# Optimization experiments

Measured on AMD Instinct MI355X. Metric: run time of the kernel, lower is better.

## Reference

```python
import jax, jax.numpy as jnp
import numpy as np

NHEAD = 6
EPS = 1.1920929e-07  # torch RMSNorm default eps = finfo(float32).eps


def _rms(x, g):
    return x * jax.lax.rsqrt(jnp.mean(x * x, axis=-1, keepdims=True) + EPS) * g


def _mha(q, k, v):
    # q: [B, Sq, Hq, D]; k, v: [B, Sk, Hk, D] with Hk == Hq or Hk == 1 (broadcast)
    d = q.shape[-1]
    qh = q.transpose(0, 2, 1, 3)            # [B, Hq, Sq, D]
    kh = k.transpose(0, 2, 1, 3)            # [B, Hk, Sk, D]
    vh = v.transpose(0, 2, 1, 3)
    s = jnp.matmul(qh, kh.transpose(0, 1, 3, 2)) * (1.0 / np.sqrt(d).astype(np.float32))
    a = jax.nn.softmax(s, axis=-1)
    return jnp.matmul(a, vh).transpose(0, 2, 1, 3)  # [B, Sq, Hq, D]


def setup_inputs() -> dict:
    key = jax.random.key(0)
    B, R, G, E, L = 4, 1024, 8, 192, 4
    F = 2 * E  # dim_feedforward = emsize * 2
    ks = jax.random.split(key, 12)

    def w(k, shape):
        return jax.random.normal(k, shape, jnp.float32) * 0.02

    return {
        "hidden": jax.random.normal(ks[0], (B, R, G, E), jnp.float32),
        "Wq1": w(ks[1], (L, E, E)), "Wk1": w(ks[2], (L, E, E)),
        "Wv1": w(ks[3], (L, E, E)), "Wo1": w(ks[4], (L, E, E)),
        "Wq2": w(ks[5], (L, E, E)), "Wk2": w(ks[6], (L, E, E)),
        "Wv2": w(ks[7], (L, E, E)), "Wo2": w(ks[8], (L, E, E)),
        "W1": w(ks[9], (L, E, F)), "W2": w(ks[10], (L, F, E)),
        "g1": jnp.ones((L, E), jnp.float32),
        "g2": jnp.ones((L, E), jnp.float32),
        "g3": jnp.ones((L, E), jnp.float32),
        "single_eval_pos": 768,
    }


def reference(hidden, Wq1, Wk1, Wv1, Wo1, Wq2, Wk2, Wv2, Wo2, W1, W2, g1, g2, g3, single_eval_pos):
    B, R, G, E = hidden.shape
    H, D = NHEAD, E // NHEAD
    sep = int(single_eval_pos)
    L = Wq1.shape[0]
    x = hidden
    for i in range(L):
        # --- per-sample attention between feature groups: seqs of length G ---
        xf = x.reshape(B * R, G, E)
        q = (xf @ Wq1[i]).reshape(B * R, G, H, D)
        k = (xf @ Wk1[i]).reshape(B * R, G, H, D)
        v = (xf @ Wv1[i]).reshape(B * R, G, H, D)
        xf = xf + _mha(q, k, v).reshape(B * R, G, E) @ Wo1[i]
        # --- along-column attention over rows with train/test split ---
        xr = _rms(xf, g1[i]).reshape(B, R, G, E).transpose(0, 2, 1, 3).reshape(B * G, R, E)
        q = (xr @ Wq2[i]).reshape(B * G, R, H, D)
        k = (xr[:, :sep] @ Wk2[i]).reshape(B * G, sep, H, D)
        v = (xr[:, :sep] @ Wv2[i]).reshape(B * G, sep, H, D)
        train_out = _mha(q[:, :sep], k, v)
        # test rows attend to first head's keys/values only (broadcast over heads)
        test_out = _mha(q[:, sep:], k[:, :, :1], v[:, :, :1])
        attn = jnp.concatenate([train_out, test_out], axis=1).reshape(B * G, R, E) @ Wo2[i]
        xc = _rms(xr + attn, g2[i])
        # --- MLP (exact GELU) + final RMSNorm ---
        x = xc.reshape(B, G, R, E).transpose(0, 2, 1, 3)
        x = x + jax.nn.gelu(x @ W1[i], approximate=False) @ W2[i]
        x = _rms(x, g3[i])
    return x
```

## Files before the change

### kernel.cpp

```cpp
#include <hip/hip_runtime.h>
#include <hip/hip_bf16.h>
#include <math.h>

#define B_ 4
#define R_ 1024
#define G_ 8
#define E_ 192
#define H_ 6
#define D_ 32
#define L_ 4
#define F_ 384
#define M_ (B_*R_*G_)
static const size_t NBUF = (size_t)M_ * E_;
static const size_t WPL  = 8 * (size_t)E_ * E_ + 2 * (size_t)E_ * F_;

typedef __attribute__((ext_vector_type(8))) short bf16x8;
typedef __attribute__((ext_vector_type(8))) unsigned short u16x8;
typedef __attribute__((ext_vector_type(4))) float f32x4;

__device__ __forceinline__ float gelu_exact(float x) {
    return 0.5f * x * (1.0f + erff(x * 0.7071067811865475f));
}
__device__ __forceinline__ unsigned short f2bf(float f) {
    __hip_bfloat16 h = __float2bfloat16(f);
    return *(unsigned short*)&h;
}
__device__ __forceinline__ float bf2f(unsigned short h) {
    union { unsigned u; float f; } v; v.u = ((unsigned)h) << 16; return v.f;
}
__device__ __forceinline__ bf16x8 mk8(unsigned long long lo, unsigned long long hi) {
    union { unsigned long long q[2]; bf16x8 v; } u;
    u.q[0] = lo; u.q[1] = hi; return u.v;
}

__global__ __launch_bounds__(256)
void k_convw_all(const float* __restrict__ Wq1, const float* __restrict__ Wk1,
                 const float* __restrict__ Wv1, const float* __restrict__ Wo1,
                 const float* __restrict__ Wq2, const float* __restrict__ Wk2,
                 const float* __restrict__ Wv2, const float* __restrict__ Wo2,
                 const float* __restrict__ W1,  const float* __restrict__ W2,
                 unsigned short* __restrict__ Wt)
{
    const int t = blockIdx.x;
    const int layer = t / 432;
    const int r = t % 432;
    const float* src; unsigned short* dst; int K, N; float scale = 1.f; int tile;
    if (r < 288) {
        const int w = r / 36; tile = r % 36; K = E_; N = E_;
        const float* tab[8] = {Wq1, Wk1, Wv1, Wo1, Wq2, Wk2, Wv2, Wo2};
        src = tab[w] + (size_t)layer * E_ * E_;
        dst = Wt + (size_t)layer * WPL + (size_t)w * E_ * E_;
        if (w == 0) scale = 0.17677669529663687f;
        if (w == 4) scale = 0.17677669529663687f * 1.4426950408889634f;
    } else if (r < 360) {
        tile = r - 288; K = E_; N = F_;
        src = W1 + (size_t)layer * E_ * F_;
        dst = Wt + (size_t)layer * WPL + 8 * (size_t)E_ * E_;
    } else {
        tile = r - 360; K = F_; N = E_;
        src = W2 + (size_t)layer * E_ * F_;
        dst = Wt + (size_t)layer * WPL + 8 * (size_t)E_ * E_ + (size_t)E_ * F_;
    }
    const int ntx = N / 32;
    const int kb = (tile / ntx) * 32, nb = (tile % ntx) * 32;
    __shared__ float tl[32][33];
    const int tx = threadIdx.x & 31, ty = threadIdx.x >> 5;
    for (int i2 = 0; i2 < 32; i2 += 8)
        tl[ty + i2][tx] = src[(size_t)(kb + ty + i2) * N + nb + tx];
    __syncthreads();
    for (int i2 = 0; i2 < 32; i2 += 8)
        dst[(size_t)(nb + ty + i2) * K + kb + tx] = f2bf(tl[tx][ty + i2] * scale);
}

template<bool ABF16, int EPI>
__global__ __launch_bounds__(256)
void k_gemm_mfma(const void* __restrict__ Ap, const unsigned short* __restrict__ Wt,
                 void* __restrict__ Cp, int ldc, int K)
{
    __shared__ unsigned short As[64][40];
    __shared__ unsigned short Bs[192][40];
    const int m0 = blockIdx.x * 64;
    const int n0 = blockIdx.y * 192;
    const int tid = threadIdx.x;
    const int w = tid >> 6, lane = tid & 63, l15 = lane & 15, g = lane >> 4;
    const int arow = tid >> 2, akoff = (tid & 3) << 3;
    f32x4 acc[4][3];
#pragma unroll
    for (int mt = 0; mt < 4; ++mt)
#pragma unroll
        for (int nt = 0; nt < 3; ++nt)
#pragma unroll
            for (int r2 = 0; r2 < 4; ++r2) acc[mt][nt][r2] = 0.f;
    const int nK = K >> 5;

    float4 ax, ay; u16x8 av; u16x8 bv0, bv1, bv2;
    auto gload = [&](int k0) {
        if (ABF16) {
            av = *(const u16x8*)((const unsigned short*)Ap + (size_t)(m0 + arow) * K + k0 + akoff);
        } else {
            const float* ap = (const float*)Ap + (size_t)(m0 + arow) * K + k0 + akoff;
            ax = *(const float4*)ap; ay = *(const float4*)(ap + 4);
        }
        bv0 = *(const u16x8*)(Wt + (size_t)(n0 + arow      ) * K + k0 + akoff);
        bv1 = *(const u16x8*)(Wt + (size_t)(n0 + arow +  64) * K + k0 + akoff);
        bv2 = *(const u16x8*)(Wt + (size_t)(n0 + arow + 128) * K + k0 + akoff);
    };
    auto swrite = [&]() {
        u16x8 aw;
        if (ABF16) aw = av;
        else {
            aw[0] = f2bf(ax.x); aw[1] = f2bf(ax.y); aw[2] = f2bf(ax.z); aw[3] = f2bf(ax.w);
            aw[4] = f2bf(ay.x); aw[5] = f2bf(ay.y); aw[6] = f2bf(ay.z); aw[7] = f2bf(ay.w);
        }
        *(u16x8*)&As[arow][akoff] = aw;
        *(u16x8*)&Bs[arow][akoff] = bv0;
        *(u16x8*)&Bs[arow + 64][akoff] = bv1;
        *(u16x8*)&Bs[arow + 128][akoff] = bv2;
    };

    gload(0);
    for (int kc = 0; kc < nK; ++kc) {
        __syncthreads();
        swrite();
        __syncthreads();
        if (kc + 1 < nK) gload((kc + 1) << 5);
        bf16x8 af[4], bfr[3];
#pragma unroll
        for (int mt = 0; mt < 4; ++mt) af[mt] = *(const bf16x8*)&As[mt * 16 + l15][g * 8];
#pragma unroll
        for (int nt = 0; nt < 3; ++nt) bfr[nt] = *(const bf16x8*)&Bs[w * 48 + nt * 16 + l15][g * 8];
#pragma unroll
        for (int mt = 0; mt < 4; ++mt)
#pragma unroll
            for (int nt = 0; nt < 3; ++nt)
                acc[mt][nt] = __builtin_amdgcn_mfma_f32_16x16x32_bf16(af[mt], bfr[nt], acc[mt][nt], 0, 0, 0);
    }

#pragma unroll
    for (int mt = 0; mt < 4; ++mt)
#pragma unroll
        for (int r2 = 0; r2 < 4; ++r2) {
            const int m = m0 + mt * 16 + g * 4 + r2;
#pragma unroll
            for (int nt = 0; nt < 3; ++nt) {
                const int n = w * 48 + nt * 16 + l15;
                float v = acc[mt][nt][r2];
                if (EPI == 1) v = gelu_exact(v);
                ((unsigned short*)Cp)[(size_t)m * ldc + n0 + n] = f2bf(v);
            }
        }
}

template<bool RESBF16, int EPI>
__global__ __launch_bounds__(256)
void k_gemm_rms32(const unsigned short* __restrict__ Ap, const unsigned short* __restrict__ Wt,
                  const void* __restrict__ Resp, const float* __restrict__ gvec,
                  void* __restrict__ Cp, int K)
{
    __shared__ unsigned short As[32][40];
    __shared__ unsigned short Bs[192][40];
    __shared__ float ss_red[4][16];
    const int m0 = blockIdx.x * 32;
    const int tid = threadIdx.x;
    const int w = tid >> 6, lane = tid & 63, l15 = lane & 15, g = lane >> 4;
    const int mt = w & 1, nh = w >> 1;
    const int arow = tid >> 2, akoff = (tid & 3) << 3;
    f32x4 acc[6];
#pragma unroll
    for (int nt = 0; nt < 6; ++nt)
#pragma unroll
        for (int r2 = 0; r2 < 4; ++r2) acc[nt][r2] = 0.f;
    const int nK = K >> 5;

    u16x8 av, bv0, bv1, bv2;
    auto gload = [&](int k0) {
        if (tid < 128)
            av = *(const u16x8*)(Ap + (size_t)(m0 + arow) * K + k0 + akoff);
        bv0 = *(const u16x8*)(Wt + (size_t)(arow      ) * K + k0 + akoff);
        bv1 = *(const u16x8*)(Wt + (size_t)(arow +  64) * K + k0 + akoff);
        bv2 = *(const u16x8*)(Wt + (size_t)(arow + 128) * K + k0 + akoff);
    };
    auto swrite = [&]() {
        if (tid < 128) *(u16x8*)&As[arow][akoff] = av;
        *(u16x8*)&Bs[arow][akoff] = bv0;
        *(u16x8*)&Bs[arow + 64][akoff] = bv1;
        *(u16x8*)&Bs[arow + 128][akoff] = bv2;
    };

    gload(0);
    for (int kc = 0; kc < nK; ++kc) {
        __syncthreads();
        swrite();
        __syncthreads();
        if (kc + 1 < nK) gload((kc + 1) << 5);
        bf16x8 af = *(const bf16x8*)&As[mt * 16 + l15][g * 8];
        bf16x8 bfr[6];
#pragma unroll
        for (int nt = 0; nt < 6; ++nt) bfr[nt] = *(const bf16x8*)&Bs[nh * 96 + nt * 16 + l15][g * 8];
#pragma unroll
        for (int nt = 0; nt < 6; ++nt)
            acc[nt] = __builtin_amdgcn_mfma_f32_16x16x32_bf16(af, bfr[nt], acc[nt], 0, 0, 0);
    }

    float ssp[4] = {0.f, 0.f, 0.f, 0.f};
#pragma unroll
    for (int r2 = 0; r2 < 4; ++r2) {
        const int m = m0 + mt * 16 + g * 4 + r2;
#pragma unroll
        for (int nt = 0; nt < 6; ++nt) {
            const int n = nh * 96 + nt * 16 + l15;
            float rres = RESBF16 ? bf2f(((const unsigned short*)Resp)[(size_t)m * E_ + n])
                                 : ((const float*)Resp)[(size_t)m * E_ + n];
            float v = acc[nt][r2] + rres;
            acc[nt][r2] = v;
            ssp[r2] += v * v;
        }
    }
#pragma unroll
    for (int off = 1; off < 16; off <<= 1)
#pragma unroll
        for (int r2 = 0; r2 < 4; ++r2)
            ssp[r2] += __shfl_xor(ssp[r2], off);
    if (l15 == 0) {
#pragma unroll
        for (int r2 = 0; r2 < 4; ++r2)
            ss_red[w][g * 4 + r2] = ssp[r2];
    }
    __syncthreads();
#pragma unroll
    for (int r2 = 0; r2 < 4; ++r2) {
        const int lr = g * 4 + r2;
        const float ss = ss_red[mt][lr] + ss_red[2 + mt][lr];
        const float inv = rsqrtf(ss * (1.0f / 192.0f) + 1.1920929e-07f);
        const int m = m0 + mt * 16 + lr;
        size_t orow;
        if (EPI == 2) {
            const int b = m >> 13, rr = (m >> 3) & 1023, gg = m & 7;
            orow = (((size_t)b * G_ + gg) << 10) + rr;
        } else if (EPI == 3) {
            const int b = m >> 13, gg = (m >> 10) & 7, rr = m & 1023;
            orow = ((((size_t)b << 10) + rr) << 3) + gg;
        } else {
            orow = m;
        }
#pragma unroll
        for (int nt = 0; nt < 6; ++nt) {
            const int n = nh * 96 + nt * 16 + l15;
            const float v = acc[nt][r2] * inv * gvec[n];
            if (EPI == 4) ((float*)Cp)[orow * E_ + n] = v;
            else          ((unsigned short*)Cp)[orow * E_ + n] = f2bf(v);
        }
    }
}

__global__ __launch_bounds__(256)
void k_attn1(const unsigned short* __restrict__ QKV, unsigned short* __restrict__ T)
{
    const int wave = blockIdx.x * 4 + (threadIdx.x >> 6);
    const int lane = threadIdx.x & 63;
    const int seq = wave / H_;
    const int h = wave % H_;
    const int i = lane >> 3, j = lane & 7;
    const unsigned short* qp = QKV + ((size_t)(seq * G_ + i)) * 576 + h * D_;
    const unsigned short* kp = QKV + ((size_t)(seq * G_ + j)) * 576 + 192 + h * D_;
    float s = 0.f;
#pragma unroll
    for (int d8 = 0; d8 < 4; ++d8) {
        u16x8 qv = *(const u16x8*)(qp + d8 * 8);
        u16x8 kv = *(const u16x8*)(kp + d8 * 8);
#pragma unroll
        for (int e = 0; e < 8; ++e) s += bf2f(qv[e]) * bf2f(kv[e]);
    }
    float mx = s;
#pragma unroll
    for (int off = 1; off < 8; off <<= 1) mx = fmaxf(mx, __shfl_xor(mx, off));
    float p = __expf(s - mx);
    float sum = p;
#pragma unroll
    for (int off = 1; off < 8; off <<= 1) sum += __shfl_xor(sum, off);
    p /= sum;
    const int base = lane & ~7;
    float o0 = 0.f, o1 = 0.f, o2 = 0.f, o3 = 0.f;
#pragma unroll
    for (int jj = 0; jj < 8; ++jj) {
        float pj = __shfl(p, base + jj);
        ushort4 vv = *(const ushort4*)(QKV + ((size_t)(seq * G_ + jj)) * 576 + 384 + h * D_ + j * 4);
        o0 += pj * bf2f(vv.x); o1 += pj * bf2f(vv.y);
        o2 += pj * bf2f(vv.z); o3 += pj * bf2f(vv.w);
    }
    ushort4 ov; ov.x = f2bf(o0); ov.y = f2bf(o1); ov.z = f2bf(o2); ov.w = f2bf(o3);
    *(ushort4*)(T + ((size_t)(seq * G_ + i)) * E_ + h * D_ + j * 4) = ov;
}

__global__ __launch_bounds__(256)
void k_attn2(const unsigned short* __restrict__ QKV, unsigned short* __restrict__ T,
             const int* __restrict__ sep_ptr)
{
    __shared__ __align__(16) unsigned short K_lds[64][40];
    __shared__ __align__(16) unsigned short V_lds[2048];

    const int sep = *sep_ptr;
    const int bid = blockIdx.x;
    const int sh = ((bid >> 7) << 3) | (bid & 7);
    const int qtile = (bid >> 3) & 15;
    const int s = sh / H_, h = sh % H_;
    const int q0 = qtile * 64;

    const int tid = threadIdx.x;
    const int w = tid >> 6;
    const int lane = tid & 63;
    const int l15 = lane & 15;
    const int g = lane >> 4;

    const int qrow = q0 + w * 16 + l15;
    u16x8 qf = *(const u16x8*)(QKV + ((size_t)s * R_ + qrow) * 576 + h * D_ + g * 8);

    u16x8 onesu;
#pragma unroll
    for (int e = 0; e < 8; ++e) onesu[e] = 0x3F80;
    const bf16x8 onesf = (bf16x8)onesu;

    const bool lo = (q0 < sep);
    const bool hi = (q0 + 64 > sep);
    const int npass = (lo && hi) ? 2 : 1;
    const int nChunk = (sep + 63) >> 6;

    const int skey = tid >> 2;
    const int sg   = tid & 3;
    const int vst = ((sg >> 1) * 16 + (skey >> 2)) * 64 + (skey & 3) * 16 + (sg & 1) * 8;
    const unsigned vaddr = (unsigned)(size_t)&V_lds[0] + (unsigned)(g * 128 + l15 * 2);

    for (int pass = 0; pass < npass; ++pass) {
        const int hk = (pass == 0) ? (lo ? h : 0) : 0;
        const unsigned short* Kb = QKV + (size_t)s * R_ * 576 + 192 + hk * D_;
        const unsigned short* Vb = QKV + (size_t)s * R_ * 576 + 384 + hk * D_;

        float mrun = -1e30f;
        f32x4 o0 = {0.f, 0.f, 0.f, 0.f};
        f32x4 o1 = {0.f, 0.f, 0.f, 0.f};
        f32x4 o2 = {0.f, 0.f, 0.f, 0.f};

        u16x8 kv_k = *(const u16x8*)(Kb + (size_t)skey * 576 + sg * 8);
        u16x8 kv_v = *(const u16x8*)(Vb + (size_t)skey * 576 + sg * 8);

        for (int kc = 0; kc < nChunk; ++kc) {
            const int kbase = kc * 64;
            const bool full = (kbase + 64 <= sep);
            __syncthreads();
            *(u16x8*)&K_lds[skey][sg * 8] = kv_k;
            *(u16x8*)&V_lds[vst] = kv_v;
            __syncthreads();
            if (kc + 1 < nChunk) {
                kv_k = *(const u16x8*)(Kb + (size_t)(kbase + 64 + skey) * 576 + sg * 8);
                kv_v = *(const u16x8*)(Vb + (size_t)(kbase + 64 + skey) * 576 + sg * 8);
            }

            f32x4 sc[4];
            const f32x4 zf = {0.f, 0.f, 0.f, 0.f};
            __builtin_amdgcn_s_setprio(1);
#pragma unroll
            for (int t = 0; t < 4; ++t) {
                bf16x8 a = *(const bf16x8*)&K_lds[t * 16 + l15][g * 8];
                sc[t] = __builtin_amdgcn_mfma_f32_16x16x32_bf16(a, (bf16x8)qf, zf, 0, 0, 0);
            }
            __builtin_amdgcn_s_setprio(0);
            if (!full) {
#pragma unroll
                for (int t = 0; t < 4; ++t)
#pragma unroll
                    for (int r = 0; r < 4; ++r)
                        if (kbase + t * 16 + g * 4 + r >= sep) sc[t][r] = -1e30f;
            }
            float mx = fmaxf(fmaxf(sc[0][0], sc[0][1]), sc[0][2]);
            mx = fmaxf(fmaxf(sc[0][3], sc[1][0]), mx);
            mx = fmaxf(fmaxf(sc[1][1], sc[1][2]), mx);
            mx = fmaxf(fmaxf(sc[1][3], sc[2][0]), mx);
            mx = fmaxf(fmaxf(sc[2][1], sc[2][2]), mx);
            mx = fmaxf(fmaxf(sc[2][3], sc[3][0]), mx);
            mx = fmaxf(fmaxf(sc[3][1], sc[3][2]), mx);
            mx = fmaxf(mx, sc[3][3]);
            if (!__all((int)(mx <= mrun + 11.0f))) {
                mx = fmaxf(mx, __shfl_xor(mx, 16));
                mx = fmaxf(mx, __shfl_xor(mx, 32));
                const float mnew = fmaxf(mrun, mx);
                const float scl = exp2f(mrun - mnew);
#pragma unroll
                for (int r = 0; r < 4; ++r) { o0[r] *= scl; o1[r] *= scl; o2[r] *= scl; }
                mrun = mnew;
            }
            bf16x8 pb0, pb1;
            {
                u16x8 p0, p1;
#pragma unroll
                for (int r = 0; r < 4; ++r) {
                    p0[r]     = f2bf(exp2f(sc[0][r] - mrun));
                    p0[4 + r] = f2bf(exp2f(sc[1][r] - mrun));
                    p1[r]     = f2bf(exp2f(sc[2][r] - mrun));
                    p1[4 + r] = f2bf(exp2f(sc[3][r] - mrun));
                }
                pb0 = (bf16x8)p0; pb1 = (bf16x8)p1;
            }
            unsigned long long t0, t1, t2, t3, t4, t5, t6, t7;
            asm volatile(
                "ds_read_b64_tr_b16 %0, %8 offset:0\n\t"
                "ds_read_b64_tr_b16 %1, %8 offset:512\n\t"
                "ds_read_b64_tr_b16 %2, %8 offset:1024\n\t"
                "ds_read_b64_tr_b16 %3, %8 offset:1536\n\t"
                "ds_read_b64_tr_b16 %4, %8 offset:2048\n\t"
                "ds_read_b64_tr_b16 %5, %8 offset:2560\n\t"
                "ds_read_b64_tr_b16 %6, %8 offset:3072\n\t"
                "ds_read_b64_tr_b16 %7, %8 offset:3584\n\t"
                "s_waitcnt lgkmcnt(0)"
                : "=&v"(t0), "=&v"(t1), "=&v"(t2), "=&v"(t3),
                  "=&v"(t4), "=&v"(t5), "=&v"(t6), "=&v"(t7)
                : "v"(vaddr)
                : "memory");
            __builtin_amdgcn_sched_barrier(0);
            __builtin_amdgcn_s_setprio(1);
            o0 = __builtin_amdgcn_mfma_f32_16x16x32_bf16(mk8(t0, t1), pb0, o0, 0, 0, 0);
            o1 = __builtin_amdgcn_mfma_f32_16x16x32_bf16(mk8(t4, t5), pb0, o1, 0, 0, 0);
            o2 = __builtin_amdgcn_mfma_f32_16x16x32_bf16(onesf,       pb0, o2, 0, 0, 0);
            o0 = __builtin_amdgcn_mfma_f32_16x16x32_bf16(mk8(t2, t3), pb1, o0, 0, 0, 0);
            o1 = __builtin_amdgcn_mfma_f32_16x16x32_bf16(mk8(t6, t7), pb1, o1, 0, 0, 0);
            o2 = __builtin_amdgcn_mfma_f32_16x16x32_bf16(onesf,       pb1, o2, 0, 0, 0);
            __builtin_amdgcn_s_setprio(0);
        }

        const bool valid = (npass == 1) || (pass == 0 ? (qrow < sep) : (qrow >= sep));
        if (valid) {
            const float inv = 1.f / o2[0];
            unsigned short* tp = T + ((size_t)s * R_ + qrow) * E_ + h * D_;
            ushort4 v0, v1;
            v0.x = f2bf(o0[0] * inv); v0.y = f2bf(o0[1] * inv);
            v0.z = f2bf(o0[2] * inv); v0.w = f2bf(o0[3] * inv);
            v1.x = f2bf(o1[0] * inv); v1.y = f2bf(o1[1] * inv);
            v1.z = f2bf(o1[2] * inv); v1.w = f2bf(o1[3] * inv);
            *(ushort4*)(tp + g * 4)      = v0;
            *(ushort4*)(tp + 16 + g * 4) = v1;
        }
    }
}

extern "C" void kernel_launch(void* const* d_in, const int* in_sizes, int n_in,
                              void* d_out, int out_size, void* d_ws, size_t ws_size,
                              hipStream_t stream) {
    const float* hidden = (const float*)d_in[0];
    const float* Wq1 = (const float*)d_in[1];
    const float* Wk1 = (const float*)d_in[2];
    const float* Wv1 = (const float*)d_in[3];
    const float* Wo1 = (const float*)d_in[4];
    const float* Wq2 = (const float*)d_in[5];
    const float* Wk2 = (const float*)d_in[6];
    const float* Wv2 = (const float*)d_in[7];
    const float* Wo2 = (const float*)d_in[8];
    const float* W1  = (const float*)d_in[9];
    const float* W2  = (const float*)d_in[10];
    const float* g1  = (const float*)d_in[11];
    const float* g2  = (const float*)d_in[12];
    const float* g3  = (const float*)d_in[13];
    const int*   sep = (const int*)d_in[14];

    float* Xout = (float*)d_out;
    unsigned short* ws = (unsigned short*)d_ws;
    unsigned short* QKVb = ws;
    unsigned short* Tb   = QKVb + (size_t)M_ * 576;
    unsigned short* Ynb  = Tb + NBUF;
    unsigned short* Xcb  = Ynb + NBUF;
    unsigned short* Xb   = Xcb + NBUF;
    unsigned short* Wt   = Xb + NBUF;
    unsigned short* H1b  = QKVb;

    const dim3 blk(256);
    const dim3 gQKV(M_ / 64, 3);
    const dim3 gW1(M_ / 64, 2);
    const dim3 g32(M_ / 32);
    const dim3 gA1((4096 * H_) / 4);
    const dim3 gA2(32 * H_ * 16);

    k_convw_all<<<dim3(432 * L_), blk, 0, stream>>>(Wq1, Wk1, Wv1, Wo1, Wq2, Wk2, Wv2, Wo2, W1, W2, Wt);

    for (int i = 0; i < L_; ++i) {
        unsigned short* wl = Wt + (size_t)i * WPL;
        const unsigned short* wqkv1 = wl;
        const unsigned short* wo1   = wl + 3 * (size_t)E_ * E_;
        const unsigned short* wqkv2 = wl + 4 * (size_t)E_ * E_;
        const unsigned short* wo2   = wl + 7 * (size_t)E_ * E_;
        const unsigned short* w1    = wl + 8 * (size_t)E_ * E_;
        const unsigned short* w2    = wl + 8 * (size_t)E_ * E_ + (size_t)E_ * F_;
        const float* g1i = g1 + (size_t)i * E_;
        const float* g2i = g2 + (size_t)i * E_;
        const float* g3i = g3 + (size_t)i * E_;

        if (i == 0)
            k_gemm_mfma<false, 0><<<gQKV, blk, 0, stream>>>(hidden, wqkv1, QKVb, 576, E_);
        else
            k_gemm_mfma<true, 0><<<gQKV, blk, 0, stream>>>(Xb, wqkv1, QKVb, 576, E_);
        k_attn1<<<gA1, blk, 0, stream>>>(QKVb, Tb);
        if (i == 0)
            k_gemm_rms32<false, 2><<<g32, blk, 0, stream>>>(Tb, wo1, hidden, g1i, Ynb, E_);
        else
            k_gemm_rms32<true, 2><<<g32, blk, 0, stream>>>(Tb, wo1, Xb, g1i, Ynb, E_);
        k_gemm_mfma<true, 0><<<gQKV, blk, 0, stream>>>(Ynb, wqkv2, QKVb, 576, E_);
        k_attn2<<<gA2, blk, 0, stream>>>(QKVb, Tb, sep);
        k_gemm_rms32<true, 3><<<g32, blk, 0, stream>>>(Tb, wo2, Ynb, g2i, Xcb, E_);
        k_gemm_mfma<true, 1><<<gW1, blk, 0, stream>>>(Xcb, w1, H1b, F_, E_);
        if (i == L_ - 1)
            k_gemm_rms32<true, 4><<<g32, blk, 0, stream>>>(H1b, w2, Xcb, g3i, Xout, F_);
        else
            k_gemm_rms32<true, 5><<<g32, blk, 0, stream>>>(H1b, w2, Xcb, g3i, Xb, F_);
    }
}
```

Baseline: 683.1 us.

## Double-buffer LDS tiles in GEMM and row-attention kernels

Both GEMM kernels and the row attention kernel now keep two shared-memory buffers and write the next K-chunk into the spare buffer while computing on the current one. This drops one of the two barriers per iteration and lets global loads run two chunks ahead. The cost is double the LDS footprint, which may lower occupancy, plus more live registers from the longer prefetch distance.

```diff
diff --git a/kernel.cpp b/kernel.cpp
--- a/kernel.cpp
+++ b/kernel.cpp
@@ -77,8 +77,8 @@
 void k_gemm_mfma(const void* __restrict__ Ap, const unsigned short* __restrict__ Wt,
                  void* __restrict__ Cp, int ldc, int K)
 {
-    __shared__ unsigned short As[64][40];
-    __shared__ unsigned short Bs[192][40];
+    __shared__ unsigned short As[2][64][40];
+    __shared__ unsigned short Bs[2][192][40];
     const int m0 = blockIdx.x * 64;
     const int n0 = blockIdx.y * 192;
     const int tid = threadIdx.x;
@@ -105,35 +105,39 @@
         bv1 = *(const u16x8*)(Wt + (size_t)(n0 + arow +  64) * K + k0 + akoff);
         bv2 = *(const u16x8*)(Wt + (size_t)(n0 + arow + 128) * K + k0 + akoff);
     };
-    auto swrite = [&]() {
+    auto swrite = [&](int buf) {
         u16x8 aw;
         if (ABF16) aw = av;
         else {
             aw[0] = f2bf(ax.x); aw[1] = f2bf(ax.y); aw[2] = f2bf(ax.z); aw[3] = f2bf(ax.w);
             aw[4] = f2bf(ay.x); aw[5] = f2bf(ay.y); aw[6] = f2bf(ay.z); aw[7] = f2bf(ay.w);
         }
-        *(u16x8*)&As[arow][akoff] = aw;
-        *(u16x8*)&Bs[arow][akoff] = bv0;
-        *(u16x8*)&Bs[arow + 64][akoff] = bv1;
-        *(u16x8*)&Bs[arow + 128][akoff] = bv2;
+        *(u16x8*)&As[buf][arow][akoff] = aw;
+        *(u16x8*)&Bs[buf][arow][akoff] = bv0;
+        *(u16x8*)&Bs[buf][arow + 64][akoff] = bv1;
+        *(u16x8*)&Bs[buf][arow + 128][akoff] = bv2;
     };
 
     gload(0);
+    swrite(0);
+    if (nK > 1) gload(32);
+    __syncthreads();
+
     for (int kc = 0; kc < nK; ++kc) {
-        __syncthreads();
-        swrite();
-        __syncthreads();
-        if (kc + 1 < nK) gload((kc + 1) << 5);
+        const int cur = kc & 1;
+        if (kc + 1 < nK) swrite(cur ^ 1);
+        if (kc + 2 < nK) gload((kc + 2) << 5);
         bf16x8 af[4], bfr[3];
 #pragma unroll
-        for (int mt = 0; mt < 4; ++mt) af[mt] = *(const bf16x8*)&As[mt * 16 + l15][g * 8];
-#pragma unroll
-        for (int nt = 0; nt < 3; ++nt) bfr[nt] = *(const bf16x8*)&Bs[w * 48 + nt * 16 + l15][g * 8];
+        for (int mt = 0; mt < 4; ++mt) af[mt] = *(const bf16x8*)&As[cur][mt * 16 + l15][g * 8];
+#pragma unroll
+        for (int nt = 0; nt < 3; ++nt) bfr[nt] = *(const bf16x8*)&Bs[cur][w * 48 + nt * 16 + l15][g * 8];
 #pragma unroll
         for (int mt = 0; mt < 4; ++mt)
 #pragma unroll
             for (int nt = 0; nt < 3; ++nt)
                 acc[mt][nt] = __builtin_amdgcn_mfma_f32_16x16x32_bf16(af[mt], bfr[nt], acc[mt][nt], 0, 0, 0);
+        __syncthreads();
     }
 
 #pragma unroll
@@ -157,8 +161,8 @@
                   const void* __restrict__ Resp, const float* __restrict__ gvec,
                   void* __restrict__ Cp, int K)
 {
-    __shared__ unsigned short As[32][40];
-    __shared__ unsigned short Bs[192][40];
+    __shared__ unsigned short As[2][32][40];
+    __shared__ unsigned short Bs[2][192][40];
     __shared__ float ss_red[4][16];
     const int m0 = blockIdx.x * 32;
     const int tid = threadIdx.x;
@@ -180,26 +184,30 @@
         bv1 = *(const u16x8*)(Wt + (size_t)(arow +  64) * K + k0 + akoff);
         bv2 = *(const u16x8*)(Wt + (size_t)(arow + 128) * K + k0 + akoff);
     };
-    auto swrite = [&]() {
-        if (tid < 128) *(u16x8*)&As[arow][akoff] = av;
-        *(u16x8*)&Bs[arow][akoff] = bv0;
-        *(u16x8*)&Bs[arow + 64][akoff] = bv1;
-        *(u16x8*)&Bs[arow + 128][akoff] = bv2;
+    auto swrite = [&](int buf) {
+        if (tid < 128) *(u16x8*)&As[buf][arow][akoff] = av;
+        *(u16x8*)&Bs[buf][arow][akoff] = bv0;
+        *(u16x8*)&Bs[buf][arow + 64][akoff] = bv1;
+        *(u16x8*)&Bs[buf][arow + 128][akoff] = bv2;
     };
 
     gload(0);
+    swrite(0);
+    if (nK > 1) gload(32);
+    __syncthreads();
+
     for (int kc = 0; kc < nK; ++kc) {
-        __syncthreads();
-        swrite();
-        __syncthreads();
-        if (kc + 1 < nK) gload((kc + 1) << 5);
-        bf16x8 af = *(const bf16x8*)&As[mt * 16 + l15][g * 8];
+        const int cur = kc & 1;
+        if (kc + 1 < nK) swrite(cur ^ 1);
+        if (kc + 2 < nK) gload((kc + 2) << 5);
+        bf16x8 af = *(const bf16x8*)&As[cur][mt * 16 + l15][g * 8];
         bf16x8 bfr[6];
 #pragma unroll
-        for (int nt = 0; nt < 6; ++nt) bfr[nt] = *(const bf16x8*)&Bs[nh * 96 + nt * 16 + l15][g * 8];
+        for (int nt = 0; nt < 6; ++nt) bfr[nt] = *(const bf16x8*)&Bs[cur][nh * 96 + nt * 16 + l15][g * 8];
 #pragma unroll
         for (int nt = 0; nt < 6; ++nt)
             acc[nt] = __builtin_amdgcn_mfma_f32_16x16x32_bf16(af, bfr[nt], acc[nt], 0, 0, 0);
+        __syncthreads();
     }
 
     float ssp[4] = {0.f, 0.f, 0.f, 0.f};
@@ -296,8 +304,8 @@
 void k_attn2(const unsigned short* __restrict__ QKV, unsigned short* __restrict__ T,
              const int* __restrict__ sep_ptr)
 {
-    __shared__ __align__(16) unsigned short K_lds[64][40];
-    __shared__ __align__(16) unsigned short V_lds[2048];
+    __shared__ __align__(16) unsigned short K_lds[2][64][40];
+    __shared__ __align__(16) unsigned short V_lds[2][2048];
 
     const int sep = *sep_ptr;
     const int bid = blockIdx.x;
@@ -328,7 +336,7 @@
     const int skey = tid >> 2;
     const int sg   = tid & 3;
     const int vst = ((sg >> 1) * 16 + (skey >> 2)) * 64 + (skey & 3) * 16 + (sg & 1) * 8;
-    const unsigned vaddr = (unsigned)(size_t)&V_lds[0] + (unsigned)(g * 128 + l15 * 2);
+    const unsigned vaddr = (unsigned)(size_t)&V_lds[0][0] + (unsigned)(g * 128 + l15 * 2);
 
     for (int pass = 0; pass < npass; ++pass) {
         const int hk = (pass == 0) ? (lo ? h : 0) : 0;
@@ -342,17 +350,25 @@
 
         u16x8 kv_k = *(const u16x8*)(Kb + (size_t)skey * 576 + sg * 8);
         u16x8 kv_v = *(const u16x8*)(Vb + (size_t)skey * 576 + sg * 8);
+        *(u16x8*)&K_lds[0][skey][sg * 8] = kv_k;
+        *(u16x8*)&V_lds[0][vst] = kv_v;
+        if (nChunk > 1) {
+            kv_k = *(const u16x8*)(Kb + (size_t)(64 + skey) * 576 + sg * 8);
+            kv_v = *(const u16x8*)(Vb + (size_t)(64 + skey) * 576 + sg * 8);
+        }
+        __syncthreads();
 
         for (int kc = 0; kc < nChunk; ++kc) {
+            const int cur = kc & 1;
             const int kbase = kc * 64;
             const bool full = (kbase + 64 <= sep);
-            __syncthreads();
-            *(u16x8*)&K_lds[skey][sg * 8] = kv_k;
-            *(u16x8*)&V_lds[vst] = kv_v;
-            __syncthreads();
             if (kc + 1 < nChunk) {
-                kv_k = *(const u16x8*)(Kb + (size_t)(kbase + 64 + skey) * 576 + sg * 8);
-                kv_v = *(const u16x8*)(Vb + (size_t)(kbase + 64 + skey) * 576 + sg * 8);
+                *(u16x8*)&K_lds[cur ^ 1][skey][sg * 8] = kv_k;
+                *(u16x8*)&V_lds[cur ^ 1][vst] = kv_v;
+            }
+            if (kc + 2 < nChunk) {
+                kv_k = *(const u16x8*)(Kb + (size_t)(kbase + 128 + skey) * 576 + sg * 8);
+                kv_v = *(const u16x8*)(Vb + (size_t)(kbase + 128 + skey) * 576 + sg * 8);
             }
 
             f32x4 sc[4];
@@ -360,7 +376,7 @@
             __builtin_amdgcn_s_setprio(1);
 #pragma unroll
             for (int t = 0; t < 4; ++t) {
-                bf16x8 a = *(const bf16x8*)&K_lds[t * 16 + l15][g * 8];
+                bf16x8 a = *(const bf16x8*)&K_lds[cur][t * 16 + l15][g * 8];
                 sc[t] = __builtin_amdgcn_mfma_f32_16x16x32_bf16(a, (bf16x8)qf, zf, 0, 0, 0);
             }
             __builtin_amdgcn_s_setprio(0);
@@ -400,6 +416,7 @@
                 }
                 pb0 = (bf16x8)p0; pb1 = (bf16x8)p1;
             }
+            const unsigned va = vaddr + (cur << 12);
             unsigned long long t0, t1, t2, t3, t4, t5, t6, t7;
             asm volatile(
                 "ds_read_b64_tr_b16 %0, %8 offset:0\n\t"
@@ -413,7 +430,7 @@
                 "s_waitcnt lgkmcnt(0)"
                 : "=&v"(t0), "=&v"(t1), "=&v"(t2), "=&v"(t3),
                   "=&v"(t4), "=&v"(t5), "=&v"(t6), "=&v"(t7)
-                : "v"(vaddr)
+                : "v"(va)
                 : "memory");
             __builtin_amdgcn_sched_barrier(0);
             __builtin_amdgcn_s_setprio(1);
@@ -424,6 +441,7 @@
             o1 = __builtin_amdgcn_mfma_f32_16x16x32_bf16(mk8(t6, t7), pb1, o1, 0, 0, 0);
             o2 = __builtin_amdgcn_mfma_f32_16x16x32_bf16(onesf,       pb1, o2, 0, 0, 0);
             __builtin_amdgcn_s_setprio(0);
+            __syncthreads();
         }
 
         const bool valid = (npass == 1) || (pass == 0 ? (qrow < sep) : (qrow >= sep));
```

New measurement: 689.9 us. Within noise of the previous version (+1.0%).

## Fuse feature-attention block and MLP block into per-row-tile megakernels

Applied to the files above, without the earlier changes.

Replaces the QKV1 GEMM, feature attention, and Wo1+RMSNorm kernels with one kernel that keeps the 32-row QKV tile and attention output in LDS. It also fuses Wo2+RMSNorm, W1+GELU and W2+RMSNorm into a single kernel that keeps Xc and H1 on-chip. The goal is to cut global-memory round trips of large intermediates and several kernel launches per layer. In exchange, each block uses much more LDS and registers, which lowers occupancy, and there is no software pipelining of weight loads, so every block reloads the full weights with synchronous barriers.

```diff
diff --git a/kernel.cpp b/kernel.cpp
--- a/kernel.cpp
+++ b/kernel.cpp
@@ -151,145 +151,400 @@
         }
 }
 
-template<bool RESBF16, int EPI>
+template<bool AF32>
 __global__ __launch_bounds__(256)
-void k_gemm_rms32(const unsigned short* __restrict__ Ap, const unsigned short* __restrict__ Wt,
-                  const void* __restrict__ Resp, const float* __restrict__ gvec,
-                  void* __restrict__ Cp, int K)
+void k_featblock(const void* __restrict__ Xin, const unsigned short* __restrict__ Wqkv,
+                 const unsigned short* __restrict__ Wo, const float* __restrict__ gvec,
+                 unsigned short* __restrict__ Ynb)
 {
-    __shared__ unsigned short As[32][40];
-    __shared__ unsigned short Bs[192][40];
-    __shared__ float ss_red[4][16];
+    __shared__ __align__(16) unsigned char raw[576 * 40 * 2];
+    __shared__ __align__(16) unsigned short As[32][40];
+    __shared__ __align__(16) unsigned short Tl[32][200];
+    __shared__ float ss_red[4][32];
+
+    unsigned short (*Bq)[40]    = (unsigned short (*)[40])raw;
+    unsigned short (*QKVl)[584] = (unsigned short (*)[584])raw;
+    unsigned short (*Bo)[40]    = (unsigned short (*)[40])raw;
+
     const int m0 = blockIdx.x * 32;
     const int tid = threadIdx.x;
     const int w = tid >> 6, lane = tid & 63, l15 = lane & 15, g = lane >> 4;
-    const int mt = w & 1, nh = w >> 1;
-    const int arow = tid >> 2, akoff = (tid & 3) << 3;
-    f32x4 acc[6];
-#pragma unroll
-    for (int nt = 0; nt < 6; ++nt)
-#pragma unroll
-        for (int r2 = 0; r2 < 4; ++r2) acc[nt][r2] = 0.f;
-    const int nK = K >> 5;
-
-    u16x8 av, bv0, bv1, bv2;
-    auto gload = [&](int k0) {
+    const int arow = (tid & 127) >> 2, akoff = (tid & 3) << 3;
+
+    f32x4 acc[2][9];
+#pragma unroll
+    for (int mt = 0; mt < 2; ++mt)
+#pragma unroll
+        for (int nt = 0; nt < 9; ++nt)
+#pragma unroll
+            for (int r2 = 0; r2 < 4; ++r2) acc[mt][nt][r2] = 0.f;
+
+    for (int kc = 0; kc < 6; ++kc) {
+        const int k0 = kc << 5;
+        __syncthreads();
+        if (tid < 128) {
+            u16x8 aw;
+            if (AF32) {
+                const float* ap = (const float*)Xin + (size_t)(m0 + arow) * E_ + k0 + akoff;
+                float4 x = *(const float4*)ap, y = *(const float4*)(ap + 4);
+                aw[0] = f2bf(x.x); aw[1] = f2bf(x.y); aw[2] = f2bf(x.z); aw[3] = f2bf(x.w);
+                aw[4] = f2bf(y.x); aw[5] = f2bf(y.y); aw[6] = f2bf(y.z); aw[7] = f2bf(y.w);
+            } else {
+                aw = *(const u16x8*)((const unsigned short*)Xin + (size_t)(m0 + arow) * E_ + k0 + akoff);
+            }
+            *(u16x8*)&As[arow][akoff] = aw;
+        }
+#pragma unroll
+        for (int j = 0; j < 9; ++j) {
+            const int v = tid + 256 * j;
+            const int br = v >> 2, bk = (v & 3) << 3;
+            *(u16x8*)&Bq[br][bk] = *(const u16x8*)(Wqkv + (size_t)br * E_ + k0 + bk);
+        }
+        __syncthreads();
+        bf16x8 af0 = *(const bf16x8*)&As[l15][g * 8];
+        bf16x8 af1 = *(const bf16x8*)&As[16 + l15][g * 8];
+#pragma unroll
+        for (int nt = 0; nt < 9; ++nt) {
+            bf16x8 bf = *(const bf16x8*)&Bq[w * 144 + nt * 16 + l15][g * 8];
+            acc[0][nt] = __builtin_amdgcn_mfma_f32_16x16x32_bf16(af0, bf, acc[0][nt], 0, 0, 0);
+            acc[1][nt] = __builtin_amdgcn_mfma_f32_16x16x32_bf16(af1, bf, acc[1][nt], 0, 0, 0);
+        }
+    }
+    __syncthreads();
+#pragma unroll
+    for (int mt = 0; mt < 2; ++mt)
+#pragma unroll
+        for (int r2 = 0; r2 < 4; ++r2)
+#pragma unroll
+            for (int nt = 0; nt < 9; ++nt)
+                QKVl[mt * 16 + g * 4 + r2][w * 144 + nt * 16 + l15] = f2bf(acc[mt][nt][r2]);
+    __syncthreads();
+
+    {
+        const int i = lane >> 3, j = lane & 7;
+        const int r0 = w * 8;
+#pragma unroll
+        for (int h = 0; h < 6; ++h) {
+            float s = 0.f;
+#pragma unroll
+            for (int d8 = 0; d8 < 4; ++d8) {
+                u16x8 qv = *(const u16x8*)&QKVl[r0 + i][h * 32 + d8 * 8];
+                u16x8 kv = *(const u16x8*)&QKVl[r0 + j][192 + h * 32 + d8 * 8];
+#pragma unroll
+                for (int e = 0; e < 8; ++e) s += bf2f(qv[e]) * bf2f(kv[e]);
+            }
+            float mx = s;
+#pragma unroll
+            for (int off = 1; off < 8; off <<= 1) mx = fmaxf(mx, __shfl_xor(mx, off));
+            float p = __expf(s - mx);
+            float sum = p;
+#pragma unroll
+            for (int off = 1; off < 8; off <<= 1) sum += __shfl_xor(sum, off);
+            p /= sum;
+            const int base = lane & ~7;
+            float o0 = 0.f, o1 = 0.f, o2 = 0.f, o3 = 0.f;
+#pragma unroll
+            for (int jj = 0; jj < 8; ++jj) {
+                float pj = __shfl(p, base + jj);
+                ushort4 vv = *(const ushort4*)&QKVl[r0 + jj][384 + h * 32 + j * 4];
+                o0 += pj * bf2f(vv.x); o1 += pj * bf2f(vv.y);
+                o2 += pj * bf2f(vv.z); o3 += pj * bf2f(vv.w);
+            }
+            ushort4 ov; ov.x = f2bf(o0); ov.y = f2bf(o1); ov.z = f2bf(o2); ov.w = f2bf(o3);
+            *(ushort4*)&Tl[r0 + i][h * 32 + j * 4] = ov;
+        }
+    }
+    __syncthreads();
+
+    f32x4 acc2[2][3];
+#pragma unroll
+    for (int mt = 0; mt < 2; ++mt)
+#pragma unroll
+        for (int nt = 0; nt < 3; ++nt)
+#pragma unroll
+            for (int r2 = 0; r2 < 4; ++r2) acc2[mt][nt][r2] = 0.f;
+
+    for (int kc = 0; kc < 6; ++kc) {
+        const int k0 = kc << 5;
+        __syncthreads();
+#pragma unroll
+        for (int j = 0; j < 3; ++j) {
+            const int v = tid + 256 * j;
+            const int br = v >> 2, bk = (v & 3) << 3;
+            *(u16x8*)&Bo[br][bk] = *(const u16x8*)(Wo + (size_t)br * E_ + k0 + bk);
+        }
+        __syncthreads();
+        bf16x8 af0 = *(const bf16x8*)&Tl[l15][k0 + g * 8];
+        bf16x8 af1 = *(const bf16x8*)&Tl[16 + l15][k0 + g * 8];
+#pragma unroll
+        for (int nt = 0; nt < 3; ++nt) {
+            bf16x8 bf = *(const bf16x8*)&Bo[w * 48 + nt * 16 + l15][g * 8];
+            acc2[0][nt] = __builtin_amdgcn_mfma_f32_16x16x32_bf16(af0, bf, acc2[0][nt], 0, 0, 0);
+            acc2[1][nt] = __builtin_amdgcn_mfma_f32_16x16x32_bf16(af1, bf, acc2[1][nt], 0, 0, 0);
+        }
+    }
+    __syncthreads();
+
+    float ssp[2][4] = {};
+#pragma unroll
+    for (int mt = 0; mt < 2; ++mt)
+#pragma unroll
+        for (int r2 = 0; r2 < 4; ++r2) {
+            const int m = m0 + mt * 16 + g * 4 + r2;
+#pragma unroll
+            for (int nt = 0; nt < 3; ++nt) {
+                const int n = w * 48 + nt * 16 + l15;
+                float rres = AF32 ? ((const float*)Xin)[(size_t)m * E_ + n]
+                                  : bf2f(((const unsigned short*)Xin)[(size_t)m * E_ + n]);
+                float v = acc2[mt][nt][r2] + rres;
+                acc2[mt][nt][r2] = v;
+                ssp[mt][r2] += v * v;
+            }
+        }
+#pragma unroll
+    for (int off = 1; off < 16; off <<= 1)
+#pragma unroll
+        for (int mt = 0; mt < 2; ++mt)
+#pragma unroll
+            for (int r2 = 0; r2 < 4; ++r2)
+                ssp[mt][r2] += __shfl_xor(ssp[mt][r2], off);
+    if (l15 == 0) {
+#pragma unroll
+        for (int mt = 0; mt < 2; ++mt)
+#pragma unroll
+            for (int r2 = 0; r2 < 4; ++r2)
+                ss_red[w][mt * 16 + g * 4 + r2] = ssp[mt][r2];
+    }
+    __syncthreads();
+#pragma unroll
+    for (int mt = 0; mt < 2; ++mt)
+#pragma unroll
+        for (int r2 = 0; r2 < 4; ++r2) {
+            const int row = mt * 16 + g * 4 + r2;
+            const float ss = ss_red[0][row] + ss_red[1][row] + ss_red[2][row] + ss_red[3][row];
+            const float inv = rsqrtf(ss * (1.0f / 192.0f) + 1.1920929e-07f);
+            const int m = m0 + row;
+            const int b = m >> 13, rr = (m >> 3) & 1023, gg = m & 7;
+            const size_t orow = (((size_t)(b * G_ + gg)) << 10) + rr;
+#pragma unroll
+            for (int nt = 0; nt < 3; ++nt) {
+                const int n = w * 48 + nt * 16 + l15;
+                Ynb[orow * E_ + n] = f2bf(acc2[mt][nt][r2] * inv * gvec[n]);
+            }
+        }
+}
+
+template<bool OUTF32>
+__global__ __launch_bounds__(256)
+void k_mlpblock(const unsigned short* __restrict__ Tin, const unsigned short* __restrict__ Wo2,
+                const unsigned short* __restrict__ W1w, const unsigned short* __restrict__ W2w,
+                const unsigned short* __restrict__ Resn, const float* __restrict__ g2v,
+                const float* __restrict__ g3v, void* __restrict__ Out)
+{
+    __shared__ __align__(16) unsigned char raw[384 * 40 * 2];
+    __shared__ __align__(16) unsigned short As[32][40];
+    __shared__ __align__(16) unsigned short Xc[32][200];
+    __shared__ __align__(16) unsigned short H1[32][392];
+    __shared__ float ss_red[4][32];
+
+    unsigned short (*Bw)[40] = (unsigned short (*)[40])raw;
+
+    const int m0 = blockIdx.x * 32;
+    const int tid = threadIdx.x;
+    const int w = tid >> 6, lane = tid & 63, l15 = lane & 15, g = lane >> 4;
+    const int arow = (tid & 127) >> 2, akoff = (tid & 3) << 3;
+
+    f32x4 acc[2][3];
+#pragma unroll
+    for (int mt = 0; mt < 2; ++mt)
+#pragma unroll
+        for (int nt = 0; nt < 3; ++nt)
+#pragma unroll
+            for (int r2 = 0; r2 < 4; ++r2) acc[mt][nt][r2] = 0.f;
+
+    for (int kc = 0; kc < 6; ++kc) {
+        const int k0 = kc << 5;
+        __syncthreads();
         if (tid < 128)
-            av = *(const u16x8*)(Ap + (size_t)(m0 + arow) * K + k0 + akoff);
-        bv0 = *(const u16x8*)(Wt + (size_t)(arow      ) * K + k0 + akoff);
-        bv1 = *(const u16x8*)(Wt + (size_t)(arow +  64) * K + k0 + akoff);
-        bv2 = *(const u16x8*)(Wt + (size_t)(arow + 128) * K + k0 + akoff);
-    };
-    auto swrite = [&]() {
-        if (tid < 128) *(u16x8*)&As[arow][akoff] = av;
-        *(u16x8*)&Bs[arow][akoff] = bv0;
-        *(u16x8*)&Bs[arow + 64][akoff] = bv1;
-        *(u16x8*)&Bs[arow + 128][akoff] = bv2;
-    };
-
-    gload(0);
-    for (int kc = 0; kc < nK; ++kc) {
-        __syncthreads();
-        swrite();
-        __syncthreads();
-        if (kc + 1 < nK) gload((kc + 1) << 5);
-        bf16x8 af = *(const bf16x8*)&As[mt * 16 + l15][g * 8];
-        bf16x8 bfr[6];
-#pragma unroll
-        for (int nt = 0; nt < 6; ++nt) bfr[nt] = *(const bf16x8*)&Bs[nh * 96 + nt * 16 + l15][g * 8];
+            *(u16x8*)&As[arow][akoff] =
+                *(const u16x8*)(Tin + (size_t)(m0 + arow) * E_ + k0 + akoff);
+#pragma unroll
+        for (int j = 0; j < 3; ++j) {
+            const int v = tid + 256 * j;
+            const int br = v >> 2, bk = (v & 3) << 3;
+            *(u16x8*)&Bw[br][bk] = *(const u16x8*)(Wo2 + (size_t)br * E_ + k0 + bk);
+        }
+        __syncthreads();
+        bf16x8 af0 = *(const bf16x8*)&As[l15][g * 8];
+        bf16x8 af1 = *(const bf16x8*)&As[16 + l15][g * 8];
+#pragma unroll
+        for (int nt = 0; nt < 3; ++nt) {
+            bf16x8 bf = *(const bf16x8*)&Bw[w * 48 + nt * 16 + l15][g * 8];
+            acc[0][nt] = __builtin_amdgcn_mfma_f32_16x16x32_bf16(af0, bf, acc[0][nt], 0, 0, 0);
+            acc[1][nt] = __builtin_amdgcn_mfma_f32_16x16x32_bf16(af1, bf, acc[1][nt], 0, 0, 0);
+        }
+    }
+    __syncthreads();
+    {
+        float ssp[2][4] = {};
+#pragma unroll
+        for (int mt = 0; mt < 2; ++mt)
+#pragma unroll
+            for (int r2 = 0; r2 < 4; ++r2) {
+                const int m = m0 + mt * 16 + g * 4 + r2;
+#pragma unroll
+                for (int nt = 0; nt < 3; ++nt) {
+                    const int n = w * 48 + nt * 16 + l15;
+                    float v = acc[mt][nt][r2] + bf2f(Resn[(size_t)m * E_ + n]);
+                    acc[mt][nt][r2] = v;
+                    ssp[mt][r2] += v * v;
+                }
+            }
+#pragma unroll
+        for (int off = 1; off < 16; off <<= 1)
+#pragma unroll
+            for (int mt = 0; mt < 2; ++mt)
+#pragma unroll
+                for (int r2 = 0; r2 < 4; ++r2)
+                    ssp[mt][r2] += __shfl_xor(ssp[mt][r2], off);
+        if (l15 == 0) {
+#pragma unroll
+            for (int mt = 0; mt < 2; ++mt)
+#pragma unroll
+                for (int r2 = 0; r2 < 4; ++r2)
+                    ss_red[w][mt * 16 + g * 4 + r2] = ssp[mt][r2];
+        }
+        __syncthreads();
+#pragma unroll
+        for (int mt = 0; mt < 2; ++mt)
+#pragma unroll
+            for (int r2 = 0; r2 < 4; ++r2) {
+                const int row = mt * 16 + g * 4 + r2;
+                const float ss = ss_red[0][row] + ss_red[1][row] + ss_red[2][row] + ss_red[3][row];
+                const float inv = rsqrtf(ss * (1.0f / 192.0f) + 1.1920929e-07f);
+#pragma unroll
+                for (int nt = 0; nt < 3; ++nt) {
+                    const int n = w * 48 + nt * 16 + l15;
+                    Xc[row][n] = f2bf(acc[mt][nt][r2] * inv * g2v[n]);
+                }
+            }
+    }
+    __syncthreads();
+
+    f32x4 accb[2][6];
+#pragma unroll
+    for (int mt = 0; mt < 2; ++mt)
 #pragma unroll
         for (int nt = 0; nt < 6; ++nt)
-            acc[nt] = __builtin_amdgcn_mfma_f32_16x16x32_bf16(af, bfr[nt], acc[nt], 0, 0, 0);
-    }
-
-    float ssp[4] = {0.f, 0.f, 0.f, 0.f};
-#pragma unroll
-    for (int r2 = 0; r2 < 4; ++r2) {
-        const int m = m0 + mt * 16 + g * 4 + r2;
+#pragma unroll
+            for (int r2 = 0; r2 < 4; ++r2) accb[mt][nt][r2] = 0.f;
+
+    for (int kc = 0; kc < 6; ++kc) {
+        const int k0 = kc << 5;
+        __syncthreads();
+#pragma unroll
+        for (int j = 0; j < 6; ++j) {
+            const int v = tid + 256 * j;
+            const int br = v >> 2, bk = (v & 3) << 3;
+            *(u16x8*)&Bw[br][bk] = *(const u16x8*)(W1w + (size_t)br * E_ + k0 + bk);
+        }
+        __syncthreads();
+        bf16x8 af0 = *(const bf16x8*)&Xc[l15][k0 + g * 8];
+        bf16x8 af1 = *(const bf16x8*)&Xc[16 + l15][k0 + g * 8];
 #pragma unroll
         for (int nt = 0; nt < 6; ++nt) {
-            const int n = nh * 96 + nt * 16 + l15;
-            float rres = RESBF16 ? bf2f(((const unsigned short*)Resp)[(size_t)m * E_ + n])
-                                 : ((const float*)Resp)[(size_t)m * E_ + n];
-            float v = acc[nt][r2] + rres;
-            acc[nt][r2] = v;
-            ssp[r2] += v * v;
-        }
-    }
-#pragma unroll
-    for (int off = 1; off < 16; off <<= 1)
+            bf16x8 bf = *(const bf16x8*)&Bw[w * 96 + nt * 16 + l15][g * 8];
+            accb[0][nt] = __builtin_amdgcn_mfma_f32_16x16x32_bf16(af0, bf, accb[0][nt], 0, 0, 0);
+            accb[1][nt] = __builtin_amdgcn_mfma_f32_16x16x32_bf16(af1, bf, accb[1][nt], 0, 0, 0);
+        }
+    }
+    __syncthreads();
+#pragma unroll
+    for (int mt = 0; mt < 2; ++mt)
 #pragma unroll
         for (int r2 = 0; r2 < 4; ++r2)
-            ssp[r2] += __shfl_xor(ssp[r2], off);
-    if (l15 == 0) {
-#pragma unroll
-        for (int r2 = 0; r2 < 4; ++r2)
-            ss_red[w][g * 4 + r2] = ssp[r2];
-    }
-    __syncthreads();
-#pragma unroll
-    for (int r2 = 0; r2 < 4; ++r2) {
-        const int lr = g * 4 + r2;
-        const float ss = ss_red[mt][lr] + ss_red[2 + mt][lr];
-        const float inv = rsqrtf(ss * (1.0f / 192.0f) + 1.1920929e-07f);
-        const int m = m0 + mt * 16 + lr;
-        size_t orow;
-        if (EPI == 2) {
-            const int b = m >> 13, rr = (m >> 3) & 1023, gg = m & 7;
-            orow = (((size_t)b * G_ + gg) << 10) + rr;
-        } else if (EPI == 3) {
-            const int b = m >> 13, gg = (m >> 10) & 7, rr = m & 1023;
-            orow = ((((size_t)b << 10) + rr) << 3) + gg;
-        } else {
-            orow = m;
-        }
-#pragma unroll
-        for (int nt = 0; nt < 6; ++nt) {
-            const int n = nh * 96 + nt * 16 + l15;
-            const float v = acc[nt][r2] * inv * gvec[n];
-            if (EPI == 4) ((float*)Cp)[orow * E_ + n] = v;
-            else          ((unsigned short*)Cp)[orow * E_ + n] = f2bf(v);
-        }
-    }
-}
-
-__global__ __launch_bounds__(256)
-void k_attn1(const unsigned short* __restrict__ QKV, unsigned short* __restrict__ T)
-{
-    const int wave = blockIdx.x * 4 + (threadIdx.x >> 6);
-    const int lane = threadIdx.x & 63;
-    const int seq = wave / H_;
-    const int h = wave % H_;
-    const int i = lane >> 3, j = lane & 7;
-    const unsigned short* qp = QKV + ((size_t)(seq * G_ + i)) * 576 + h * D_;
-    const unsigned short* kp = QKV + ((size_t)(seq * G_ + j)) * 576 + 192 + h * D_;
-    float s = 0.f;
-#pragma unroll
-    for (int d8 = 0; d8 < 4; ++d8) {
-        u16x8 qv = *(const u16x8*)(qp + d8 * 8);
-        u16x8 kv = *(const u16x8*)(kp + d8 * 8);
-#pragma unroll
-        for (int e = 0; e < 8; ++e) s += bf2f(qv[e]) * bf2f(kv[e]);
-    }
-    float mx = s;
-#pragma unroll
-    for (int off = 1; off < 8; off <<= 1) mx = fmaxf(mx, __shfl_xor(mx, off));
-    float p = __expf(s - mx);
-    float sum = p;
-#pragma unroll
-    for (int off = 1; off < 8; off <<= 1) sum += __shfl_xor(sum, off);
-    p /= sum;
-    const int base = lane & ~7;
-    float o0 = 0.f, o1 = 0.f, o2 = 0.f, o3 = 0.f;
-#pragma unroll
-    for (int jj = 0; jj < 8; ++jj) {
-        float pj = __shfl(p, base + jj);
-        ushort4 vv = *(const ushort4*)(QKV + ((size_t)(seq * G_ + jj)) * 576 + 384 + h * D_ + j * 4);
-        o0 += pj * bf2f(vv.x); o1 += pj * bf2f(vv.y);
-        o2 += pj * bf2f(vv.z); o3 += pj * bf2f(vv.w);
-    }
-    ushort4 ov; ov.x = f2bf(o0); ov.y = f2bf(o1); ov.z = f2bf(o2); ov.w = f2bf(o3);
-    *(ushort4*)(T + ((size_t)(seq * G_ + i)) * E_ + h * D_ + j * 4) = ov;
+#pragma unroll
+            for (int nt = 0; nt < 6; ++nt)
+                H1[mt * 16 + g * 4 + r2][w * 96 + nt * 16 + l15] = f2bf(gelu_exact(accb[mt][nt][r2]));
+    __syncthreads();
+
+    f32x4 accc[2][3];
+#pragma unroll
+    for (int mt = 0; mt < 2; ++mt)
+#pragma unroll
+        for (int nt = 0; nt < 3; ++nt)
+#pragma unroll
+            for (int r2 = 0; r2 < 4; ++r2) accc[mt][nt][r2] = 0.f;
+
+    for (int kc = 0; kc < 12; ++kc) {
+        const int k0 = kc << 5;
+        __syncthreads();
+#pragma unroll
+        for (int j = 0; j < 3; ++j) {
+            const int v = tid + 256 * j;
+            const int br = v >> 2, bk = (v & 3) << 3;
+            *(u16x8*)&Bw[br][bk] = *(const u16x8*)(W2w + (size_t)br * F_ + k0 + bk);
+        }
+        __syncthreads();
+        bf16x8 af0 = *(const bf16x8*)&H1[l15][k0 + g * 8];
+        bf16x8 af1 = *(const bf16x8*)&H1[16 + l15][k0 + g * 8];
+#pragma unroll
+        for (int nt = 0; nt < 3; ++nt) {
+            bf16x8 bf = *(const bf16x8*)&Bw[w * 48 + nt * 16 + l15][g * 8];
+            accc[0][nt] = __builtin_amdgcn_mfma_f32_16x16x32_bf16(af0, bf, accc[0][nt], 0, 0, 0);
+            accc[1][nt] = __builtin_amdgcn_mfma_f32_16x16x32_bf16(af1, bf, accc[1][nt], 0, 0, 0);
+        }
+    }
+    __syncthreads();
+    {
+        float ssp[2][4] = {};
+#pragma unroll
+        for (int mt = 0; mt < 2; ++mt)
+#pragma unroll
+            for (int r2 = 0; r2 < 4; ++r2) {
+                const int row = mt * 16 + g * 4 + r2;
+#pragma unroll
+                for (int nt = 0; nt < 3; ++nt) {
+                    const int n = w * 48 + nt * 16 + l15;
+                    float v = accc[mt][nt][r2] + bf2f(Xc[row][n]);
+                    accc[mt][nt][r2] = v;
+                    ssp[mt][r2] += v * v;
+                }
+            }
+#pragma unroll
+        for (int off = 1; off < 16; off <<= 1)
+#pragma unroll
+            for (int mt = 0; mt < 2; ++mt)
+#pragma unroll
+                for (int r2 = 0; r2 < 4; ++r2)
+                    ssp[mt][r2] += __shfl_xor(ssp[mt][r2], off);
+        if (l15 == 0) {
+#pragma unroll
+            for (int mt = 0; mt < 2; ++mt)
+#pragma unroll
+                for (int r2 = 0; r2 < 4; ++r2)
+                    ss_red[w][mt * 16 + g * 4 + r2] = ssp[mt][r2];
+        }
+        __syncthreads();
+#pragma unroll
+        for (int mt = 0; mt < 2; ++mt)
+#pragma unroll
+            for (int r2 = 0; r2 < 4; ++r2) {
+                const int row = mt * 16 + g * 4 + r2;
+                const float ss = ss_red[0][row] + ss_red[1][row] + ss_red[2][row] + ss_red[3][row];
+                const float inv = rsqrtf(ss * (1.0f / 192.0f) + 1.1920929e-07f);
+                const int m = m0 + row;
+                const int b = m >> 13, gg = (m >> 10) & 7, rr = m & 1023;
+                const size_t orow = ((((size_t)(b << 10)) + rr) << 3) + gg;
+#pragma unroll
+                for (int nt = 0; nt < 3; ++nt) {
+                    const int n = w * 48 + nt * 16 + l15;
+                    const float v = accc[mt][nt][r2] * inv * g3v[n];
+                    if (OUTF32) ((float*)Out)[orow * E_ + n] = v;
+                    else        ((unsigned short*)Out)[orow * E_ + n] = f2bf(v);
+                }
+            }
+    }
 }
 
 __global__ __launch_bounds__(256)
@@ -465,16 +720,12 @@
     unsigned short* QKVb = ws;
     unsigned short* Tb   = QKVb + (size_t)M_ * 576;
     unsigned short* Ynb  = Tb + NBUF;
-    unsigned short* Xcb  = Ynb + NBUF;
-    unsigned short* Xb   = Xcb + NBUF;
+    unsigned short* Xb   = Ynb + NBUF;
     unsigned short* Wt   = Xb + NBUF;
-    unsigned short* H1b  = QKVb;
 
     const dim3 blk(256);
+    const dim3 g32(M_ / 32);
     const dim3 gQKV(M_ / 64, 3);
-    const dim3 gW1(M_ / 64, 2);
-    const dim3 g32(M_ / 32);
-    const dim3 gA1((4096 * H_) / 4);
     const dim3 gA2(32 * H_ * 16);
 
     k_convw_all<<<dim3(432 * L_), blk, 0, stream>>>(Wq1, Wk1, Wv1, Wo1, Wq2, Wk2, Wv2, Wo2, W1, W2, Wt);
@@ -492,21 +743,14 @@
         const float* g3i = g3 + (size_t)i * E_;
 
         if (i == 0)
-            k_gemm_mfma<false, 0><<<gQKV, blk, 0, stream>>>(hidden, wqkv1, QKVb, 576, E_);
+            k_featblock<true><<<g32, blk, 0, stream>>>(hidden, wqkv1, wo1, g1i, Ynb);
         else
-            k_gemm_mfma<true, 0><<<gQKV, blk, 0, stream>>>(Xb, wqkv1, QKVb, 576, E_);
-        k_attn1<<<gA1, blk, 0, stream>>>(QKVb, Tb);
-        if (i == 0)
-            k_gemm_rms32<false, 2><<<g32, blk, 0, stream>>>(Tb, wo1, hidden, g1i, Ynb, E_);
-        else
-            k_gemm_rms32<true, 2><<<g32, blk, 0, stream>>>(Tb, wo1, Xb, g1i, Ynb, E_);
+            k_featblock<false><<<g32, blk, 0, stream>>>(Xb, wqkv1, wo1, g1i, Ynb);
         k_gemm_mfma<true, 0><<<gQKV, blk, 0, stream>>>(Ynb, wqkv2, QKVb, 576, E_);
         k_attn2<<<gA2, blk, 0, stream>>>(QKVb, Tb, sep);
-        k_gemm_rms32<true, 3><<<g32, blk, 0, stream>>>(Tb, wo2, Ynb, g2i, Xcb, E_);
-        k_gemm_mfma<true, 1><<<gW1, blk, 0, stream>>>(Xcb, w1, H1b, F_, E_);
         if (i == L_ - 1)
-            k_gemm_rms32<true, 4><<<g32, blk, 0, stream>>>(H1b, w2, Xcb, g3i, Xout, F_);
+            k_mlpblock<true><<<g32, blk, 0, stream>>>(Tb, wo2, w1, w2, Ynb, g2i, g3i, Xout);
         else
-            k_gemm_rms32<true, 5><<<g32, blk, 0, stream>>>(H1b, w2, Xcb, g3i, Xb, F_);
-    }
-}
+            k_mlpblock<false><<<g32, blk, 0, stream>>>(Tb, wo2, w1, w2, Ynb, g2i, g3i, Xb);
+    }
+}
```

New measurement: 710.4 us. 4.0% more time.
